# Kernel optimization log

Hardware: AMD Instinct MI355X
Metric: run time of the kernel (lower is better)

The kernel has to match this reference:

```python
import jax, jax.numpy as jnp
import numpy as np

B, CH, H, W = 32, 128, 32, 32
EMB = 64      # embedding_dim
NEMB = 8192   # codebook size


def setup_inputs() -> dict:
    key = jax.random.key(0)
    k1, k2, k3, k4 = jax.random.split(key, 4)
    z = jax.random.normal(k1, (B, CH, H, W), jnp.float32)
    # 1x1 conv == per-pixel linear: weight [EMB, CH], bias [EMB]
    proj_w = jax.random.normal(k2, (EMB, CH), jnp.float32) * 0.05
    proj_b = jax.random.normal(k3, (EMB,), jnp.float32) * 0.01
    embed_w = jax.random.normal(k4, (NEMB, EMB), jnp.float32)
    return {"z": z, "proj_w": proj_w, "proj_b": proj_b, "embed_w": embed_w}


def reference(z, proj_w, proj_b, embed_w):
    Bz, C, Hh, Ww = z.shape
    sg = jax.lax.stop_gradient
    # 1x1 conv then permute(0,2,3,1): [B,C,H,W] -> [B,H,W,E]
    z_e = jnp.einsum('bchw,ec->bhwe', z, proj_w) + proj_b
    flat = z_e.reshape(-1, z_e.shape[-1])  # [N, E], N = B*H*W
    dist = ((flat * flat).sum(1, keepdims=True)
            - 2.0 * (flat @ embed_w.T)
            + (embed_w * embed_w).sum(1)[None, :])
    z_q_ind = jnp.argmin(dist, axis=1).reshape(Bz, Hh, Ww)  # argmax(-dist)
    z_q_emb = embed_w[z_q_ind]  # gather: [B,H,W,E]
    commitment_cost = 0.25
    kld_scale = 10.0
    latent_loss = kld_scale * (
        commitment_cost * jnp.mean((sg(z_q_emb) - z_e) ** 2)
        + jnp.mean((z_q_emb - sg(z_e)) ** 2))
    z_q_flat = z_q_emb
    # straight-through estimator
    z_q_st = z_e + sg(z_q_emb - z_e)
    out = jnp.transpose(z_q_st, (0, 3, 1, 2))  # [B,E,H,W]
    return out, z_q_flat, latent_loss, z_q_ind
```

## Files before the change

kernel.cpp:

```cpp
#include <hip/hip_runtime.h>

#define NPIX   32768
#define NEMB_  8192
#define EMB_   64
#define CH_    128
#define CAPP   768

#define OUT_OFF  0
#define ZQ_OFF   2097152
#define LOSS_OFF 4194304
#define IND_OFF  4194305

typedef _Float16 h8   __attribute__((ext_vector_type(8)));
typedef float    f16f __attribute__((ext_vector_type(16)));

__global__ __launch_bounds__(256) void k_wpack(
    const float* __restrict__ ew, const float* __restrict__ pw,
    float4* __restrict__ W4, float* __restrict__ pwT,
    float* __restrict__ wsq, float* __restrict__ wsqp,
    float* __restrict__ lacc, int* __restrict__ done)
{
    const int tid = threadIdx.x;
    {
        const int i = blockIdx.x * 256 + tid;
        const float v = pw[i];
        const int e = i >> 7, c = i & 127;
        pwT[c * 64 + e] = v;
    }
    const int m = blockIdx.x * 256 + tid;
    const float4* wr = (const float4*)(ew + (size_t)m * EMB_);
    float w[EMB_];
    float s = 0.f;
    #pragma unroll
    for (int i = 0; i < 16; i++) {
        float4 v = wr[i];
        w[4*i] = v.x; w[4*i+1] = v.y; w[4*i+2] = v.z; w[4*i+3] = v.w;
        s += v.x*v.x + v.y*v.y + v.z*v.z + v.w*v.w;
    }
    wsq[m] = s;
    float sh = (float)(_Float16)s;
    float sl = s - sh;
    const int t  = m >> 5;
    const int li = m & 31;
    #pragma unroll
    for (int s5 = 0; s5 < 4; s5++) {
        #pragma unroll
        for (int h = 0; h < 2; h++) {
            h8 hh;
            #pragma unroll
            for (int j = 0; j < 8; j++) hh[j] = (_Float16)w[s5 * 16 + h * 8 + j];
            W4[(size_t)(t * 5 + s5) * 64 + h * 32 + li] = __builtin_bit_cast(float4, hh);
        }
    }
    {
        h8 hh;
        #pragma unroll
        for (int j = 0; j < 8; j++) hh[j] = (_Float16)0.f;
        hh[0] = (_Float16)sh; hh[1] = (_Float16)sl;
        W4[(size_t)(t * 5 + 4) * 64 + 0 * 32 + li] = __builtin_bit_cast(float4, hh);
        #pragma unroll
        for (int j = 0; j < 8; j++) hh[j] = (_Float16)0.f;
        W4[(size_t)(t * 5 + 4) * 64 + 1 * 32 + li] = __builtin_bit_cast(float4, hh);
    }
    __shared__ float red[256];
    red[tid] = s;
    __syncthreads();
    for (int o = 128; o > 0; o >>= 1) {
        if (tid < o) red[tid] = fmaxf(red[tid], red[tid + o]);
        __syncthreads();
    }
    if (tid == 0) wsqp[blockIdx.x] = red[0];
    if (blockIdx.x == 0 && tid == 0) { *lacc = 0.f; *done = 0; }
}

__device__ __forceinline__ unsigned long long pack_key(float d, int m)
{
    unsigned fb = __float_as_uint(d);
    fb ^= ((int)fb < 0) ? 0xFFFFFFFFu : 0x80000000u;
    return ((unsigned long long)fb << 32) | (unsigned)m;
}

__global__ __launch_bounds__(1024, 4) void k_fused3(
    const float4* __restrict__ W4, const float* __restrict__ z,
    const float* __restrict__ pwT, const float* __restrict__ pb,
    const float* __restrict__ wsqp, const float* __restrict__ wsq,
    const float* __restrict__ ew,
    float* __restrict__ out, float* __restrict__ lacc, int* __restrict__ done)
{
    __shared__ __align__(16) float xs[128][68];
    __shared__ float s1s[2048], s2s[2048], s3s[2048];
    __shared__ short i1s[2048], i2s[2048];
    __shared__ float xsqp_s[8][128];
    __shared__ float thr_s[128];
    __shared__ int   pairs[CAPP];
    __shared__ unsigned long long pbest[128];
    __shared__ int   winner_s[128];
    __shared__ int   smask[128];
    __shared__ float wred[16];
    __shared__ int   npair_s;
    __shared__ float wm_s;

    const int tid  = threadIdx.x;
    const int wv   = tid >> 6;
    const int lane = tid & 63;
    const int n0   = blockIdx.x * 128;
    const int hlf  = lane >> 5;

    if (tid == 0) npair_s = 0;
    if (tid < 128) { smask[tid] = 0; pbest[tid] = ~0ULL; }
    if (tid < 32) {
        float w = wsqp[tid];
        #pragma unroll
        for (int o = 16; o > 0; o >>= 1) w = fmaxf(w, __shfl_xor(w, o));
        if (tid == 0) wm_s = w;
    }

    {
        const int oct = tid >> 7;
        const int pxp = tid & 127;
        const int e0  = __builtin_amdgcn_readfirstlane(oct << 3);
        const float* zp = z + (size_t)(n0 >> 10) * (CH_ * 1024) + (n0 & 1023) + pxp;
        float acc[8];
        #pragma unroll
        for (int j = 0; j < 8; j++) acc[j] = 0.f;
        #pragma unroll 8
        for (int c = 0; c < CH_; c++) {
            const float zv = zp[(size_t)c * 1024];
            const float4* wr = (const float4*)(pwT + c * 64 + e0);
            float4 w0 = wr[0], w1 = wr[1];
            acc[0] = fmaf(zv, w0.x, acc[0]); acc[1] = fmaf(zv, w0.y, acc[1]);
            acc[2] = fmaf(zv, w0.z, acc[2]); acc[3] = fmaf(zv, w0.w, acc[3]);
            acc[4] = fmaf(zv, w1.x, acc[4]); acc[5] = fmaf(zv, w1.y, acc[5]);
            acc[6] = fmaf(zv, w1.z, acc[6]); acc[7] = fmaf(zv, w1.w, acc[7]);
        }
        const float4* pb4 = (const float4*)(pb + e0);
        float4 b0 = pb4[0], b1 = pb4[1];
        acc[0] += b0.x; acc[1] += b0.y; acc[2] += b0.z; acc[3] += b0.w;
        acc[4] += b1.x; acc[5] += b1.y; acc[6] += b1.z; acc[7] += b1.w;
        float sq = 0.f;
        #pragma unroll
        for (int j = 0; j < 8; j++) sq += acc[j] * acc[j];
        ((float4*)&xs[pxp][0])[oct * 2]     = make_float4(acc[0], acc[1], acc[2], acc[3]);
        ((float4*)&xs[pxp][0])[oct * 2 + 1] = make_float4(acc[4], acc[5], acc[6], acc[7]);
        xsqp_s[oct][pxp] = sq;
    }
    __syncthreads();

    h8 bfr[4][5];
    #pragma unroll
    for (int j = 0; j < 4; j++) {
        const int px = j * 32 + (lane & 31);
        #pragma unroll
        for (int s5 = 0; s5 < 4; s5++) {
            float4 u0 = *(const float4*)(&xs[px][s5 * 16 + hlf * 8]);
            float4 u1 = *(const float4*)(&xs[px][s5 * 16 + hlf * 8 + 4]);
            h8 hh;
            hh[0]=(_Float16)u0.x; hh[1]=(_Float16)u0.y; hh[2]=(_Float16)u0.z; hh[3]=(_Float16)u0.w;
            hh[4]=(_Float16)u1.x; hh[5]=(_Float16)u1.y; hh[6]=(_Float16)u1.z; hh[7]=(_Float16)u1.w;
            bfr[j][s5] = hh;
        }
        h8 hh;
        #pragma unroll
        for (int q = 0; q < 8; q++) hh[q] = (_Float16)0.f;
        if (hlf == 0) { hh[0] = (_Float16)-0.5f; hh[1] = (_Float16)-0.5f; }
        bfr[j][4] = hh;
    }

    const f16f kzero = {0,0,0,0,0,0,0,0,0,0,0,0,0,0,0,0};
    float s1[4], s2[4], s3[4];
    int   i1[4], i2[4];
    #pragma unroll
    for (int j = 0; j < 4; j++) { s1[j]=s2[j]=s3[j]=-3.0e38f; i1[j]=i2[j]=0; }

    const int tb = wv * 16;
    const float4* Wb = W4 + (size_t)tb * 320 + lane;
    float4 A[5];
    #pragma unroll
    for (int s = 0; s < 5; s++) A[s] = Wb[s * 64];

#define REDUCE_J(ACC, JJ)                                                      \
    {                                                                          \
        float t0 = fmaxf(fmaxf(ACC[0],  ACC[1]),  ACC[2]);                     \
        float t1 = fmaxf(fmaxf(ACC[3],  ACC[4]),  ACC[5]);                     \
        float t2 = fmaxf(fmaxf(ACC[6],  ACC[7]),  ACC[8]);                     \
        float t3 = fmaxf(fmaxf(ACC[9],  ACC[10]), ACC[11]);                    \
        float t4 = fmaxf(fmaxf(ACC[12], ACC[13]), ACC[14]);                    \
        float v  = fmaxf(fmaxf(fmaxf(t0, t1), fmaxf(t2, t3)),                  \
                         fmaxf(t4, ACC[15]));                                  \
        v = fmaxf(v, __shfl_xor(v, 32));                                       \
        bool c1 = v > s1[JJ];                                                  \
        bool c2 = v > s2[JJ];                                                  \
        int  cand = c1 ? i1[JJ] : gt;                                          \
        i2[JJ] = c2 ? cand : i2[JJ];                                           \
        s3[JJ] = fmaxf(fminf(s2[JJ], v), s3[JJ]);                              \
        s3[JJ] = fminf(s3[JJ], fmaxf(s2[JJ], v));                              \
        s2[JJ] = fmaxf(fminf(s1[JJ], v), fminf(s2[JJ], fmaxf(s1[JJ], v)));     \
        i1[JJ] = c1 ? gt : i1[JJ];                                             \
        s1[JJ] = fmaxf(s1[JJ], v);                                             \
    }

    for (int tt = 0; tt < 16; tt++) {
        const int gt = tb + tt;
        f16f acc0 = __builtin_amdgcn_mfma_f32_32x32x16_f16(
            __builtin_bit_cast(h8, A[0]), bfr[0][0], kzero, 0, 0, 0);
        f16f acc1 = __builtin_amdgcn_mfma_f32_32x32x16_f16(
            __builtin_bit_cast(h8, A[0]), bfr[1][0], kzero, 0, 0, 0);
        #pragma unroll
        for (int s = 1; s < 5; s++) {
            h8 a = __builtin_bit_cast(h8, A[s]);
            acc0 = __builtin_amdgcn_mfma_f32_32x32x16_f16(a, bfr[0][s], acc0, 0, 0, 0);
            acc1 = __builtin_amdgcn_mfma_f32_32x32x16_f16(a, bfr[1][s], acc1, 0, 0, 0);
        }
        REDUCE_J(acc0, 0)
        REDUCE_J(acc1, 1)
        f16f acc2 = __builtin_amdgcn_mfma_f32_32x32x16_f16(
            __builtin_bit_cast(h8, A[0]), bfr[2][0], kzero, 0, 0, 0);
        f16f acc3 = __builtin_amdgcn_mfma_f32_32x32x16_f16(
            __builtin_bit_cast(h8, A[0]), bfr[3][0], kzero, 0, 0, 0);
        #pragma unroll
        for (int s = 1; s < 5; s++) {
            h8 a = __builtin_bit_cast(h8, A[s]);
            acc2 = __builtin_amdgcn_mfma_f32_32x32x16_f16(a, bfr[2][s], acc2, 0, 0, 0);
            acc3 = __builtin_amdgcn_mfma_f32_32x32x16_f16(a, bfr[3][s], acc3, 0, 0, 0);
        }
        {
            const int tp = (tt + 1) < 16 ? (tt + 1) : 15;
            const float4* wp = Wb + (size_t)tp * 320;
            #pragma unroll
            for (int s = 0; s < 5; s++) A[s] = wp[s * 64];
        }
        REDUCE_J(acc2, 2)
        REDUCE_J(acc3, 3)
    }
#undef REDUCE_J

    if (lane < 32) {
        #pragma unroll
        for (int j = 0; j < 4; j++) {
            const int cell = (j * 32 + lane) * 16 + wv;
            s1s[cell] = s1[j]; s2s[cell] = s2[j]; s3s[cell] = s3[j];
            i1s[cell] = (short)i1[j]; i2s[cell] = (short)i2[j];
        }
    }
    __syncthreads();

    if (tid < 128) {
        float s1g = s1s[tid * 16];
        #pragma unroll
        for (int c = 1; c < 16; c++) s1g = fmaxf(s1g, s1s[tid * 16 + c]);
        float xq = xsqp_s[0][tid];
        #pragma unroll
        for (int o = 1; o < 8; o++) xq += xsqp_s[o][tid];
        float E = 0.00125f * sqrtf(xq * wm_s) + 1e-5f * wm_s + 3e-4f;
        thr_s[tid] = s1g - 2.0f * E;
    }
    __syncthreads();
    #pragma unroll
    for (int k = 0; k < 2; k++) {
        const int cell = k * 1024 + tid;
        const int px = cell >> 4, ch = cell & 15;
        const float th = thr_s[px];
        const float cs1 = s1s[cell], cs2 = s2s[cell], cs3 = s3s[cell];
        if (cs3 >= th) {
            int pos = atomicAdd(&npair_s, 16);
            if (pos + 16 <= CAPP) {
                for (int t = 0; t < 16; t++)
                    pairs[pos + t] = (px << 8) | (ch * 16 + t);
            } else {
                for (int t = 0; t < 16; t++)
                    if (pos + t < CAPP) pairs[pos + t] = -1;
                smask[px] = 1;
            }
        } else {
            if (cs1 >= th) {
                int pos = atomicAdd(&npair_s, 1);
                if (pos < CAPP) pairs[pos] = (px << 8) | (int)i1s[cell];
                else smask[px] = 1;
            }
            if (cs2 >= th) {
                int pos = atomicAdd(&npair_s, 1);
                if (pos < CAPP) pairs[pos] = (px << 8) | (int)i2s[cell];
                else smask[px] = 1;
            }
        }
    }
    __syncthreads();
    const int np = npair_s < CAPP ? npair_s : CAPP;

    const int lg = lane >> 4;
    const int ld = lane & 15;
    for (int i = wv; i < np; i += 16) {
        const int pr = pairs[i];
        if (pr < 0) continue;
        const int p = pr >> 8;
        if (smask[p]) continue;
        const int t = pr & 255;
        const float4* tb4 = (const float4*)(ew + (size_t)t * 2048);
        float4 wq[8];
        #pragma unroll
        for (int q = 0; q < 8; q++) wq[q] = tb4[q * 64 + lane];
        const float4 xq = *(const float4*)(&xs[p][ld * 4]);
        unsigned long long best = ~0ULL;
        #pragma unroll
        for (int q = 0; q < 8; q++) {
            float dp = wq[q].x*xq.x + wq[q].y*xq.y + wq[q].z*xq.z + wq[q].w*xq.w;
            dp += __shfl_xor(dp, 1);
            dp += __shfl_xor(dp, 2);
            dp += __shfl_xor(dp, 4);
            dp += __shfl_xor(dp, 8);
            const int m = t * 32 + q * 4 + lg;
            unsigned long long key = pack_key(fmaf(-2.f, dp, wsq[m]), m);
            best = key < best ? key : best;
        }
        { unsigned long long o = __shfl_xor(best, 16); best = o < best ? o : best; }
        { unsigned long long o = __shfl_xor(best, 32); best = o < best ? o : best; }
        if (lane == 0) atomicMin(&pbest[p], best);
    }
    for (int p = wv; p < 128; p += 16) {
        if (!smask[p]) continue;
        const float4 xq = *(const float4*)(&xs[p][ld * 4]);
        unsigned long long bk = ~0ULL;
        for (int t = 0; t < 256; t++) {
            const float4* tb4 = (const float4*)(ew + (size_t)t * 2048);
            #pragma unroll
            for (int q = 0; q < 8; q++) {
                float4 wv4 = tb4[q * 64 + lane];
                float dp = wv4.x*xq.x + wv4.y*xq.y + wv4.z*xq.z + wv4.w*xq.w;
                dp += __shfl_xor(dp, 1);
                dp += __shfl_xor(dp, 2);
                dp += __shfl_xor(dp, 4);
                dp += __shfl_xor(dp, 8);
                const int m = t * 32 + q * 4 + lg;
                unsigned long long key = pack_key(fmaf(-2.f, dp, wsq[m]), m);
                bk = key < bk ? key : bk;
            }
        }
        { unsigned long long o = __shfl_xor(bk, 16); bk = o < bk ? o : bk; }
        { unsigned long long o = __shfl_xor(bk, 32); bk = o < bk ? o : bk; }
        if (lane == 0) atomicMin(&pbest[p], bk);
    }
    __syncthreads();
    if (tid < 128) {
        const int win = (int)(unsigned)(pbest[tid] & 0xFFFFFFFFULL);
        winner_s[tid] = win;
        out[IND_OFF + n0 + tid] = (float)win;
    }
    __syncthreads();
    float lsum = 0.f;
    {
        const int px = tid >> 3, sg = tid & 7;
        const int win = winner_s[px];
        const float4* wr = (const float4*)(ew + (size_t)win * EMB_ + sg * 8);
        float4* xr  = (float4*)(&xs[px][sg * 8]);
        float4* zq4 = (float4*)(out + ZQ_OFF + (size_t)(n0 + px) * EMB_ + sg * 8);
        #pragma unroll
        for (int i = 0; i < 2; i++) {
            float4 w4v = wr[i];
            float4 z4  = xr[i];
            float d0 = w4v.x - z4.x, d1 = w4v.y - z4.y;
            float d2 = w4v.z - z4.z, d3 = w4v.w - z4.w;
            lsum += d0*d0 + d1*d1 + d2*d2 + d3*d3;
            xr[i]  = w4v;
            zq4[i] = w4v;
        }
    }
    __syncthreads();
    {
        const int bI  = n0 >> 10;
        const int hw0 = n0 & 1023;
        float* ob = out + OUT_OFF + (size_t)bI * (EMB_ * 1024) + hw0;
        #pragma unroll
        for (int r = 0; r < 8; r++) {
            const int idx = r * 1024 + tid;
            const int e = idx >> 7, px = idx & 127;
            ob[(size_t)e * 1024 + px] = xs[px][e];
        }
    }
    {
        float v = lsum;
        #pragma unroll
        for (int o = 1; o < 64; o <<= 1) v += __shfl_xor(v, o);
        if (lane == 0) wred[wv] = v;
    }
    __syncthreads();
    if (tid == 0) {
        float s = wred[0];
        #pragma unroll
        for (int k = 1; k < 16; k++) s += wred[k];
        atomicAdd(lacc, s);
        __threadfence();
        int old = atomicAdd(done, 1);
        if (old == (int)gridDim.x - 1) {
            float tot = atomicAdd(lacc, 0.0f);
            out[LOSS_OFF] = 12.5f * (tot / 2097152.0f);
        }
    }
}

extern "C" void kernel_launch(void* const* d_in, const int* in_sizes, int n_in,
                              void* d_out, int out_size, void* d_ws, size_t ws_size,
                              hipStream_t stream)
{
    const float* z  = (const float*)d_in[0];
    const float* pw = (const float*)d_in[1];
    const float* pb = (const float*)d_in[2];
    const float* ew = (const float*)d_in[3];
    float* out = (float*)d_out;

    char* ws = (char*)d_ws;
    float4* W4   = (float4*)(ws);
    float*  pwT  = (float*) (ws + 1310720);
    float*  wsq  = (float*) (ws + 1474560);
    float*  wsqp = (float*) (ws + 1507328);
    float*  lacc = (float*) (ws + 1507456);
    int*    done = (int*)   (ws + 1507460);

    hipLaunchKernelGGL(k_wpack,  dim3(32),  dim3(256), 0, stream,
                       ew, pw, W4, pwT, wsq, wsqp, lacc, done);
    hipLaunchKernelGGL(k_fused3, dim3(256), dim3(1024), 0, stream,
                       W4, z, pwT, pb, wsqp, wsq, ew, out, lacc, done);
}
```

Before: 189.6 us.

## Split waves into pixel groups with 32-tile codebook chunks per wave

Each wave now covers 64 pixels (two 32-pixel B fragments) over 32 codebook tiles instead of all 128 pixels over 16 tiles. The wave grid becomes 8 codebook chunks by 2 pixel groups, which halves the per-wave fragment registers and top-3 state. It also shrinks the shared candidate arrays and the cell-scan loop. The cost is twice as many codebook A-fragment loads per wave, coarser chunks of 32 when a near-tie forces a full-chunk re-check (more exact-check pairs, more overflow risk), and fewer MFMAs between loads to hide latency.

```diff
diff --git a/kernel.cpp b/kernel.cpp
--- a/kernel.cpp
+++ b/kernel.cpp
@@ -88,8 +88,8 @@
     float* __restrict__ out, float* __restrict__ lacc, int* __restrict__ done)
 {
     __shared__ __align__(16) float xs[128][68];
-    __shared__ float s1s[2048], s2s[2048], s3s[2048];
-    __shared__ short i1s[2048], i2s[2048];
+    __shared__ float s1s[1024], s2s[1024], s3s[1024];
+    __shared__ short i1s[1024], i2s[1024];
     __shared__ float xsqp_s[8][128];
     __shared__ float thr_s[128];
     __shared__ int   pairs[CAPP];
@@ -146,10 +146,13 @@
     }
     __syncthreads();
 
-    h8 bfr[4][5];
+    const int ch = wv & 7;
+    const int pg = wv >> 3;
+
+    h8 bfr[2][4];
     #pragma unroll
-    for (int j = 0; j < 4; j++) {
-        const int px = j * 32 + (lane & 31);
+    for (int j = 0; j < 2; j++) {
+        const int px = pg * 64 + j * 32 + (lane & 31);
         #pragma unroll
         for (int s5 = 0; s5 < 4; s5++) {
             float4 u0 = *(const float4*)(&xs[px][s5 * 16 + hlf * 8]);
@@ -159,26 +162,29 @@
             hh[4]=(_Float16)u1.x; hh[5]=(_Float16)u1.y; hh[6]=(_Float16)u1.z; hh[7]=(_Float16)u1.w;
             bfr[j][s5] = hh;
         }
+    }
+    h8 btail;
+    {
         h8 hh;
         #pragma unroll
         for (int q = 0; q < 8; q++) hh[q] = (_Float16)0.f;
         if (hlf == 0) { hh[0] = (_Float16)-0.5f; hh[1] = (_Float16)-0.5f; }
-        bfr[j][4] = hh;
+        btail = hh;
     }
 
     const f16f kzero = {0,0,0,0,0,0,0,0,0,0,0,0,0,0,0,0};
-    float s1[4], s2[4], s3[4];
-    int   i1[4], i2[4];
+    float s1[2], s2[2], s3[2];
+    int   i1[2], i2[2];
     #pragma unroll
-    for (int j = 0; j < 4; j++) { s1[j]=s2[j]=s3[j]=-3.0e38f; i1[j]=i2[j]=0; }
-
-    const int tb = wv * 16;
+    for (int j = 0; j < 2; j++) { s1[j]=s2[j]=s3[j]=-3.0e38f; i1[j]=i2[j]=0; }
+
+    const int tb = ch * 32;
     const float4* Wb = W4 + (size_t)tb * 320 + lane;
     float4 A[5];
     #pragma unroll
     for (int s = 0; s < 5; s++) A[s] = Wb[s * 64];
 
-#define REDUCE_J(ACC, JJ)                                                      \
+#define REDUCE_J(ACC, JJ, GT)                                                  \
     {                                                                          \
         float t0 = fmaxf(fmaxf(ACC[0],  ACC[1]),  ACC[2]);                     \
         float t1 = fmaxf(fmaxf(ACC[3],  ACC[4]),  ACC[5]);                     \
@@ -190,54 +196,49 @@
         v = fmaxf(v, __shfl_xor(v, 32));                                       \
         bool c1 = v > s1[JJ];                                                  \
         bool c2 = v > s2[JJ];                                                  \
-        int  cand = c1 ? i1[JJ] : gt;                                          \
+        int  cand = c1 ? i1[JJ] : (GT);                                        \
         i2[JJ] = c2 ? cand : i2[JJ];                                           \
         s3[JJ] = fmaxf(fminf(s2[JJ], v), s3[JJ]);                              \
         s3[JJ] = fminf(s3[JJ], fmaxf(s2[JJ], v));                              \
         s2[JJ] = fmaxf(fminf(s1[JJ], v), fminf(s2[JJ], fmaxf(s1[JJ], v)));     \
-        i1[JJ] = c1 ? gt : i1[JJ];                                             \
+        i1[JJ] = c1 ? (GT) : i1[JJ];                                           \
         s1[JJ] = fmaxf(s1[JJ], v);                                             \
     }
 
-    for (int tt = 0; tt < 16; tt++) {
+    for (int tt = 0; tt < 32; tt++) {
         const int gt = tb + tt;
         f16f acc0 = __builtin_amdgcn_mfma_f32_32x32x16_f16(
             __builtin_bit_cast(h8, A[0]), bfr[0][0], kzero, 0, 0, 0);
+        #pragma unroll
+        for (int s = 1; s < 4; s++)
+            acc0 = __builtin_amdgcn_mfma_f32_32x32x16_f16(
+                __builtin_bit_cast(h8, A[s]), bfr[0][s], acc0, 0, 0, 0);
+        acc0 = __builtin_amdgcn_mfma_f32_32x32x16_f16(
+            __builtin_bit_cast(h8, A[4]), btail, acc0, 0, 0, 0);
+        REDUCE_J(acc0, 0, gt)
         f16f acc1 = __builtin_amdgcn_mfma_f32_32x32x16_f16(
             __builtin_bit_cast(h8, A[0]), bfr[1][0], kzero, 0, 0, 0);
         #pragma unroll
-        for (int s = 1; s < 5; s++) {
-            h8 a = __builtin_bit_cast(h8, A[s]);
-            acc0 = __builtin_amdgcn_mfma_f32_32x32x16_f16(a, bfr[0][s], acc0, 0, 0, 0);
-            acc1 = __builtin_amdgcn_mfma_f32_32x32x16_f16(a, bfr[1][s], acc1, 0, 0, 0);
-        }
-        REDUCE_J(acc0, 0)
-        REDUCE_J(acc1, 1)
-        f16f acc2 = __builtin_amdgcn_mfma_f32_32x32x16_f16(
-            __builtin_bit_cast(h8, A[0]), bfr[2][0], kzero, 0, 0, 0);
-        f16f acc3 = __builtin_amdgcn_mfma_f32_32x32x16_f16(
-            __builtin_bit_cast(h8, A[0]), bfr[3][0], kzero, 0, 0, 0);
-        #pragma unroll
-        for (int s = 1; s < 5; s++) {
-            h8 a = __builtin_bit_cast(h8, A[s]);
-            acc2 = __builtin_amdgcn_mfma_f32_32x32x16_f16(a, bfr[2][s], acc2, 0, 0, 0);
-            acc3 = __builtin_amdgcn_mfma_f32_32x32x16_f16(a, bfr[3][s], acc3, 0, 0, 0);
-        }
+        for (int s = 1; s < 4; s++)
+            acc1 = __builtin_amdgcn_mfma_f32_32x32x16_f16(
+                __builtin_bit_cast(h8, A[s]), bfr[1][s], acc1, 0, 0, 0);
+        acc1 = __builtin_amdgcn_mfma_f32_32x32x16_f16(
+            __builtin_bit_cast(h8, A[4]), btail, acc1, 0, 0, 0);
         {
-            const int tp = (tt + 1) < 16 ? (tt + 1) : 15;
+            const int tp = (tt + 1) < 32 ? (tt + 1) : 31;
             const float4* wp = Wb + (size_t)tp * 320;
             #pragma unroll
             for (int s = 0; s < 5; s++) A[s] = wp[s * 64];
         }
-        REDUCE_J(acc2, 2)
-        REDUCE_J(acc3, 3)
+        REDUCE_J(acc1, 1, gt)
     }
 #undef REDUCE_J
 
     if (lane < 32) {
         #pragma unroll
-        for (int j = 0; j < 4; j++) {
-            const int cell = (j * 32 + lane) * 16 + wv;
+        for (int j = 0; j < 2; j++) {
+            const int px = pg * 64 + j * 32 + lane;
+            const int cell = px * 8 + ch;
             s1s[cell] = s1[j]; s2s[cell] = s2[j]; s3s[cell] = s3[j];
             i1s[cell] = (short)i1[j]; i2s[cell] = (short)i2[j];
         }
@@ -245,9 +246,9 @@
     __syncthreads();
 
     if (tid < 128) {
-        float s1g = s1s[tid * 16];
-        #pragma unroll
-        for (int c = 1; c < 16; c++) s1g = fmaxf(s1g, s1s[tid * 16 + c]);
+        float s1g = s1s[tid * 8];
+        #pragma unroll
+        for (int c = 1; c < 8; c++) s1g = fmaxf(s1g, s1s[tid * 8 + c]);
         float xq = xsqp_s[0][tid];
         #pragma unroll
         for (int o = 1; o < 8; o++) xq += xsqp_s[o][tid];
@@ -255,19 +256,18 @@
         thr_s[tid] = s1g - 2.0f * E;
     }
     __syncthreads();
-    #pragma unroll
-    for (int k = 0; k < 2; k++) {
-        const int cell = k * 1024 + tid;
-        const int px = cell >> 4, ch = cell & 15;
+    {
+        const int cell = tid;
+        const int px = cell >> 3, chh = cell & 7;
         const float th = thr_s[px];
         const float cs1 = s1s[cell], cs2 = s2s[cell], cs3 = s3s[cell];
         if (cs3 >= th) {
-            int pos = atomicAdd(&npair_s, 16);
-            if (pos + 16 <= CAPP) {
-                for (int t = 0; t < 16; t++)
-                    pairs[pos + t] = (px << 8) | (ch * 16 + t);
+            int pos = atomicAdd(&npair_s, 32);
+            if (pos + 32 <= CAPP) {
+                for (int t = 0; t < 32; t++)
+                    pairs[pos + t] = (px << 8) | (chh * 32 + t);
             } else {
-                for (int t = 0; t < 16; t++)
+                for (int t = 0; t < 32; t++)
                     if (pos + t < CAPP) pairs[pos + t] = -1;
                 smask[px] = 1;
             }
```

Result: faster. 156.5 us (-17.5%).
